# Performance work log

Hardware: AMD Instinct MI355X
Metric: run time of the kernel (lower is better)

## Reference

```python
import jax, jax.numpy as jnp
from jax import lax
import numpy as np

N_LAYER = 2
SEQ, BATCH, D = 4096, 32, 512


def setup_inputs() -> dict:
    key = jax.random.key(0)
    k1, k2, k3 = jax.random.split(key, 3)
    x = jax.random.normal(k1, (SEQ, BATCH, D), dtype=jnp.float32)
    # repo init: weight_ih ~ N(0, 0.01)
    W_ih = jax.random.normal(k2, (N_LAYER, D, D), dtype=jnp.float32) * 0.01
    # recurrent weight in [0,1) keeps the long ReLU recurrence bounded
    w_hh = jax.random.uniform(k3, (N_LAYER, D), dtype=jnp.float32)
    b_ih = jnp.zeros((N_LAYER, D), dtype=jnp.float32)
    return {"x": x, "W_ih": W_ih, "w_hh": w_hh, "b_ih": b_ih}


def _indrnn_layer(x, W, w, b):
    # x: (T, B, in), W: (H, in), w,b: (H,)
    proj = jnp.einsum('tbi,hi->tbh', x, W) + b  # one batched GEMM up front

    def step(h, p):
        h = jax.nn.relu(p + w * h)
        return h, h

    h0 = jnp.zeros((x.shape[1], W.shape[0]), dtype=x.dtype)
    hT, ys = lax.scan(step, h0, proj)
    return ys, hT


def reference(x, W_ih, w_hh, b_ih):
    hiddens = []
    out = x
    for l in range(W_ih.shape[0]):  # small fixed layer loop
        out, hT = _indrnn_layer(out, W_ih[l], w_hh[l], b_ih[l])
        hiddens.append(hT)
    h_n = jnp.stack(hiddens, axis=0)  # (n_layer, B, H)
    return out, h_n
```

## Files before the change

### kernel.cpp

```cpp
#include <hip/hip_runtime.h>

#define T_SEQ   4096
#define BATCH   32
#define DIM     512
#define MROWS   (T_SEQ * BATCH)
#define S_STRIDE (BATCH * DIM)
#define OUT_ELEMS ((size_t)T_SEQ * BATCH * DIM)
#define NCH     32
#define CLEN    (T_SEQ / NCH)
#define NCHAIN  (BATCH * DIM)
#define NWG     ((MROWS / 128) * (DIM / 128))

typedef __bf16 bf8_t __attribute__((ext_vector_type(8)));
typedef float  f4_t  __attribute__((ext_vector_type(4)));
typedef unsigned short u16x8 __attribute__((ext_vector_type(8)));
typedef __attribute__((address_space(1))) void gvoid_t;
typedef __attribute__((address_space(3))) void lvoid_t;

__device__ __forceinline__ unsigned short f2bf(float f) {
    unsigned int u = __float_as_uint(f);
    u += 0x7FFFu + ((u >> 16) & 1u);
    return (unsigned short)(u >> 16);
}
__device__ __forceinline__ float bf2f(unsigned short b) {
    return __uint_as_float(((unsigned int)b) << 16);
}

__global__ __launch_bounds__(256) void k_cvt(const float* __restrict__ in,
                                             unsigned short* __restrict__ out) {
    size_t i = ((size_t)blockIdx.x * 256 + threadIdx.x) * 8;
    float4 a = *reinterpret_cast<const float4*>(in + i);
    float4 b = *reinterpret_cast<const float4*>(in + i + 4);
    u16x8 o;
    o[0] = f2bf(a.x); o[1] = f2bf(a.y); o[2] = f2bf(a.z); o[3] = f2bf(a.w);
    o[4] = f2bf(b.x); o[5] = f2bf(b.y); o[6] = f2bf(b.z); o[7] = f2bf(b.w);
    *reinterpret_cast<u16x8*>(out + i) = o;
}

template <int AF32>
__global__ __launch_bounds__(256)
void k_gemm_bt(const void* __restrict__ Ap,
               const unsigned short* __restrict__ B,
               unsigned short* __restrict__ C) {
    __shared__ unsigned short As[128 * 32];
    __shared__ unsigned short Bs[128 * 32];

    const int tid  = threadIdx.x;
    const int lane = tid & 63;
    const int wv   = tid >> 6;
    const int wr   = wv >> 1;
    const int wc   = wv & 1;

    const int flat = blockIdx.x;
    const int s    = (flat & 7) * (NWG / 8) + (flat >> 3);
    const size_t gm = (size_t)(s >> 2) * 128;
    const int    gn = (s & 3) * 128;

    const int srow = tid >> 2;
    const int skk  = (tid & 3) * 8;

    f4_t acc[4][4] = {};

    const int l15 = lane & 15;
    const int lk  = (lane >> 4) * 8;

    for (int k0 = 0; k0 < 512; k0 += 32) {
#pragma unroll
        for (int i = 0; i < 2; ++i) {
            const unsigned short* gb = B + (size_t)(gn + i * 64 + srow) * 512 + k0 + skk;
            __builtin_amdgcn_global_load_lds((gvoid_t*)gb, (lvoid_t*)&Bs[i * 2048 + wv * 512], 16, 0, 0);
            if constexpr (AF32) {
                const float* ga = (const float*)Ap + (gm + (size_t)(i * 64 + srow)) * 512 + k0 + skk;
                float4 a0 = *reinterpret_cast<const float4*>(ga);
                float4 a1 = *reinterpret_cast<const float4*>(ga + 4);
                u16x8 o;
                o[0] = f2bf(a0.x); o[1] = f2bf(a0.y); o[2] = f2bf(a0.z); o[3] = f2bf(a0.w);
                o[4] = f2bf(a1.x); o[5] = f2bf(a1.y); o[6] = f2bf(a1.z); o[7] = f2bf(a1.w);
                *reinterpret_cast<u16x8*>(&As[i * 2048 + tid * 8]) = o;
            } else {
                const unsigned short* ga = (const unsigned short*)Ap + (gm + (size_t)(i * 64 + srow)) * 512 + k0 + skk;
                __builtin_amdgcn_global_load_lds((gvoid_t*)ga, (lvoid_t*)&As[i * 2048 + wv * 512], 16, 0, 0);
            }
        }
        __syncthreads();

        bf8_t af[4], bfz[4];
#pragma unroll
        for (int m = 0; m < 4; ++m)
            af[m] = *reinterpret_cast<const bf8_t*>(&As[(wr * 64 + m * 16 + l15) * 32 + lk]);
#pragma unroll
        for (int n = 0; n < 4; ++n)
            bfz[n] = *reinterpret_cast<const bf8_t*>(&Bs[(wc * 64 + n * 16 + l15) * 32 + lk]);
#pragma unroll
        for (int m = 0; m < 4; ++m)
#pragma unroll
            for (int n = 0; n < 4; ++n)
                acc[m][n] = __builtin_amdgcn_mfma_f32_16x16x32_bf16(af[m], bfz[n], acc[m][n], 0, 0, 0);
        __syncthreads();
    }

    const int crow0 = (lane >> 4) * 4;
#pragma unroll
    for (int m = 0; m < 4; ++m)
#pragma unroll
        for (int n = 0; n < 4; ++n) {
            const size_t row0 = gm + (size_t)(wr * 64 + m * 16 + crow0);
            const int    col  = gn + wc * 64 + n * 16 + l15;
#pragma unroll
            for (int r = 0; r < 4; ++r)
                C[(row0 + r) * 512 + col] = f2bf(acc[m][n][r]);
        }
}

__global__ __launch_bounds__(256)
void k_scan_p1(const unsigned short* __restrict__ q,
               const float* __restrict__ w_hh,
               const float* __restrict__ b_ih,
               float* __restrict__ Asum,
               float* __restrict__ Bsum) {
    const int g = (blockIdx.x & 63) * 256 + threadIdx.x;
    const int c = blockIdx.x >> 6;
    const float w  = w_hh[g & 511];
    const float bs = b_ih[g & 511];
    const unsigned short* p = q + (size_t)c * CLEN * S_STRIDE + g;

    float A = 0.f, Bv = 0.f;
    float s0[8], s1[8];
#pragma unroll
    for (int j = 0; j < 8; ++j) s0[j] = bf2f(p[(size_t)j * S_STRIDE]);
#pragma unroll
    for (int j = 0; j < 8; ++j) s1[j] = bf2f(p[(size_t)(8 + j) * S_STRIDE]);

    for (int j0 = 0; j0 < CLEN; j0 += 16) {
#pragma unroll
        for (int j = 0; j < 8; ++j) {
            float qv = s0[j] + bs;
            A  = fmaxf(fmaf(w, A, qv), 0.f);
            Bv = fmaf(w, Bv, qv);
        }
        if (j0 + 16 < CLEN) {
#pragma unroll
            for (int j = 0; j < 8; ++j) s0[j] = bf2f(p[(size_t)(j0 + 16 + j) * S_STRIDE]);
        }
#pragma unroll
        for (int j = 0; j < 8; ++j) {
            float qv = s1[j] + bs;
            A  = fmaxf(fmaf(w, A, qv), 0.f);
            Bv = fmaf(w, Bv, qv);
        }
        if (j0 + 24 < CLEN) {
#pragma unroll
            for (int j = 0; j < 8; ++j) s1[j] = bf2f(p[(size_t)(j0 + 24 + j) * S_STRIDE]);
        }
    }
    Asum[(size_t)c * NCHAIN + g] = A;
    Bsum[(size_t)c * NCHAIN + g] = Bv;
}

template <int MODE>
__global__ __launch_bounds__(256)
void k_scan_p2(const unsigned short* __restrict__ q,
               const float* __restrict__ w_hh,
               const float* __restrict__ b_ih,
               const float* __restrict__ Asum,
               const float* __restrict__ Bsum,
               float* __restrict__ of32,
               unsigned short* __restrict__ ob16,
               float* __restrict__ hT) {
    const int g = (blockIdx.x & 63) * 256 + threadIdx.x;
    const int c = blockIdx.x >> 6;
    const float w  = w_hh[g & 511];
    const float bs = b_ih[g & 511];

    float cw = w;
#pragma unroll
    for (int i = 0; i < 7; ++i) cw *= cw;
    float h = 0.f;
    for (int cc = 0; cc < c; ++cc)
        h = fmaxf(Asum[(size_t)cc * NCHAIN + g], fmaf(cw, h, Bsum[(size_t)cc * NCHAIN + g]));

    const size_t base = (size_t)c * CLEN * S_STRIDE + g;
    const unsigned short* p = q + base;

    float s0[8], s1[8];
#pragma unroll
    for (int j = 0; j < 8; ++j) s0[j] = bf2f(p[(size_t)j * S_STRIDE]);
#pragma unroll
    for (int j = 0; j < 8; ++j) s1[j] = bf2f(p[(size_t)(8 + j) * S_STRIDE]);

    for (int j0 = 0; j0 < CLEN; j0 += 16) {
#pragma unroll
        for (int j = 0; j < 8; ++j) {
            h = fmaxf(fmaf(w, h, s0[j] + bs), 0.f);
            const size_t idx = base + (size_t)(j0 + j) * S_STRIDE;
            if (MODE == 0) of32[idx] = h; else ob16[idx] = f2bf(h);
        }
        if (j0 + 16 < CLEN) {
#pragma unroll
            for (int j = 0; j < 8; ++j) s0[j] = bf2f(p[(size_t)(j0 + 16 + j) * S_STRIDE]);
        }
#pragma unroll
        for (int j = 0; j < 8; ++j) {
            h = fmaxf(fmaf(w, h, s1[j] + bs), 0.f);
            const size_t idx = base + (size_t)(j0 + 8 + j) * S_STRIDE;
            if (MODE == 0) of32[idx] = h; else ob16[idx] = f2bf(h);
        }
        if (j0 + 24 < CLEN) {
#pragma unroll
            for (int j = 0; j < 8; ++j) s1[j] = bf2f(p[(size_t)(j0 + 24 + j) * S_STRIDE]);
        }
    }
    if (c == NCH - 1) hT[g] = h;
}

extern "C" void kernel_launch(void* const* d_in, const int* in_sizes, int n_in,
                              void* d_out, int out_size, void* d_ws, size_t ws_size,
                              hipStream_t stream) {
    const float* x    = (const float*)d_in[0];
    const float* W_ih = (const float*)d_in[1];
    const float* w_hh = (const float*)d_in[2];
    const float* b_ih = (const float*)d_in[3];

    unsigned short* proj2 = (unsigned short*)d_ws;
    unsigned short* Wb    = proj2 + OUT_ELEMS;
    float* Asum = (float*)(Wb + 2 * 512 * 512);
    float* Bsum = Asum + (size_t)NCH * NCHAIN;

    unsigned short* proj1 = (unsigned short*)d_out;
    unsigned short* ys1   = proj1 + OUT_ELEMS;
    float* out = (float*)d_out;
    float* hT  = out + OUT_ELEMS;

    const int sgrid = 64 * NCH;

    k_cvt<<<524288 / 8 / 256, 256, 0, stream>>>(W_ih, Wb);
    k_gemm_bt<1><<<NWG, 256, 0, stream>>>(x, Wb, proj1);
    k_scan_p1<<<sgrid, 256, 0, stream>>>(proj1, w_hh, b_ih, Asum, Bsum);
    k_scan_p2<1><<<sgrid, 256, 0, stream>>>(proj1, w_hh, b_ih, Asum, Bsum,
                                            nullptr, ys1, hT);
    k_gemm_bt<0><<<NWG, 256, 0, stream>>>(ys1, Wb + 512 * 512, proj2);
    k_scan_p1<<<sgrid, 256, 0, stream>>>(proj2, w_hh + DIM, b_ih + DIM, Asum, Bsum);
    k_scan_p2<0><<<sgrid, 256, 0, stream>>>(proj2, w_hh + DIM, b_ih + DIM, Asum, Bsum,
                                            out, nullptr, hT + NCHAIN);
}
```

Measured before the change: 469.1 us.

## Restructure projection GEMM into full-N persistent tiles with double-buffered swizzled LDS

Replaces the 128x128-tile GEMM with 256 workgroups of 512 threads. Each workgroup computes full 512-wide output rows for four consecutive 128-row M tiles. The whole 512-column B slice for each K step is staged into 160KB of dynamic LDS, double-buffered with a prefetch distance of two and XOR-swizzled to avoid bank conflicts, with explicit vmcnt/lgkmcnt waits. This aims to cut redundant A reloads and barrier overhead and to overlap loads with MFMA, at the cost of heavy LDS use that limits occupancy and of fragile hand-tuned wait counts.

```diff
diff --git a/kernel.cpp b/kernel.cpp
--- a/kernel.cpp
+++ b/kernel.cpp
@@ -9,7 +9,13 @@
 #define NCH     32
 #define CLEN    (T_SEQ / NCH)
 #define NCHAIN  (BATCH * DIM)
-#define NWG     ((MROWS / 128) * (DIM / 128))
+
+#define NSTEP   32
+#define A0S     0
+#define A1S     8192
+#define B0S     16384
+#define B1S     49152
+#define GLDS_B  163840
 
 typedef __bf16 bf8_t __attribute__((ext_vector_type(8)));
 typedef float  f4_t  __attribute__((ext_vector_type(4)));
@@ -25,6 +31,9 @@
 __device__ __forceinline__ float bf2f(unsigned short b) {
     return __uint_as_float(((unsigned int)b) << 16);
 }
+
+#define VMC(n)  asm volatile("s_waitcnt vmcnt(" #n ")" ::: "memory")
+#define LGKM0   asm volatile("s_waitcnt lgkmcnt(0)" ::: "memory")
 
 __global__ __launch_bounds__(256) void k_cvt(const float* __restrict__ in,
                                              unsigned short* __restrict__ out) {
@@ -38,78 +47,159 @@
 }
 
 template <int AF32>
-__global__ __launch_bounds__(256)
-void k_gemm_bt(const void* __restrict__ Ap,
-               const unsigned short* __restrict__ B,
+__global__ __launch_bounds__(512, 2)
+void k_gemm_fn(const void* __restrict__ Ap,
+               const unsigned short* __restrict__ Bp,
                unsigned short* __restrict__ C) {
-    __shared__ unsigned short As[128 * 32];
-    __shared__ unsigned short Bs[128 * 32];
+    extern __shared__ unsigned short lds[];
 
     const int tid  = threadIdx.x;
     const int lane = tid & 63;
     const int wv   = tid >> 6;
-    const int wr   = wv >> 1;
-    const int wc   = wv & 1;
-
-    const int flat = blockIdx.x;
-    const int s    = (flat & 7) * (NWG / 8) + (flat >> 3);
-    const size_t gm = (size_t)(s >> 2) * 128;
-    const int    gn = (s & 3) * 128;
-
-    const int srow = tid >> 2;
-    const int skk  = (tid & 3) * 8;
-
-    f4_t acc[4][4] = {};
-
-    const int l15 = lane & 15;
-    const int lk  = (lane >> 4) * 8;
-
-    for (int k0 = 0; k0 < 512; k0 += 32) {
-#pragma unroll
-        for (int i = 0; i < 2; ++i) {
-            const unsigned short* gb = B + (size_t)(gn + i * 64 + srow) * 512 + k0 + skk;
-            __builtin_amdgcn_global_load_lds((gvoid_t*)gb, (lvoid_t*)&Bs[i * 2048 + wv * 512], 16, 0, 0);
+    const int l15  = lane & 15;
+    const int l16  = lane >> 4;
+    const int lj   = lane >> 3;
+    const int ss8  = lane & 7;
+    const int mbase = blockIdx.x * 4;
+
+    const unsigned short* Ab = (const unsigned short*)Ap;
+    const float*          Af = (const float*)Ap;
+
+    auto stageB = [&](int reg, int kt) {
+#pragma unroll
+        for (int j = 0; j < 8; ++j) {
+            const int r = j * 64 + wv * 8 + lj;
+            const unsigned short* src = Bp + (size_t)r * 512 + kt * 64 + (ss8 ^ lj) * 8;
+            unsigned short* dst = &lds[reg + (j * 64 + wv * 8) * 64];
+            __builtin_amdgcn_global_load_lds((gvoid_t*)src, (lvoid_t*)dst, 16, 0, 0);
+        }
+    };
+    auto stageA = [&](int reg, int kt, size_t gm) {
+#pragma unroll
+        for (int j = 0; j < 2; ++j) {
+            const int r = j * 64 + wv * 8 + lj;
+            const unsigned short* src = Ab + (gm + r) * 512 + kt * 64 + (ss8 ^ lj) * 8;
+            unsigned short* dst = &lds[reg + (j * 64 + wv * 8) * 64];
+            __builtin_amdgcn_global_load_lds((gvoid_t*)src, (lvoid_t*)dst, 16, 0, 0);
+        }
+    };
+    const int ra = tid >> 2, sg = tid & 3;
+    auto loadAf = [&](float4* h, int kt, size_t gm) {
+        const float* src = Af + (gm + ra) * 512 + kt * 64 + sg * 16;
+#pragma unroll
+        for (int q = 0; q < 4; ++q) h[q] = *reinterpret_cast<const float4*>(src + q * 4);
+    };
+    auto writeAf = [&](int reg, const float4* h) {
+        u16x8 o0, o1;
+        o0[0] = f2bf(h[0].x); o0[1] = f2bf(h[0].y); o0[2] = f2bf(h[0].z); o0[3] = f2bf(h[0].w);
+        o0[4] = f2bf(h[1].x); o0[5] = f2bf(h[1].y); o0[6] = f2bf(h[1].z); o0[7] = f2bf(h[1].w);
+        o1[0] = f2bf(h[2].x); o1[1] = f2bf(h[2].y); o1[2] = f2bf(h[2].z); o1[3] = f2bf(h[2].w);
+        o1[4] = f2bf(h[3].x); o1[5] = f2bf(h[3].y); o1[6] = f2bf(h[3].z); o1[7] = f2bf(h[3].w);
+        const int sl0 = (sg * 2) ^ (ra & 7), sl1 = (sg * 2 + 1) ^ (ra & 7);
+        *reinterpret_cast<u16x8*>(&lds[reg + ra * 64 + sl0 * 8]) = o0;
+        *reinterpret_cast<u16x8*>(&lds[reg + ra * 64 + sl1 * 8]) = o1;
+    };
+
+    f4_t  acc[8][4] = {};
+    float4 afP[4], afQ[4];
+
+    if constexpr (AF32) {
+        loadAf(afP, 0, (size_t)mbase * 128);
+        stageB(B0S, 0);
+        loadAf(afQ, 1, (size_t)mbase * 128);
+        stageB(B1S, 1);
+        VMC(20);
+        writeAf(A0S, afP);
+        LGKM0; __builtin_amdgcn_sched_barrier(0);
+        VMC(12);
+    } else {
+        stageA(A0S, 0, (size_t)mbase * 128);
+        stageB(B0S, 0);
+        stageA(A1S, 1, (size_t)mbase * 128);
+        stageB(B1S, 1);
+        VMC(10);
+    }
+    __builtin_amdgcn_s_barrier();
+
+#pragma unroll 2
+    for (int s = 0; s < NSTEP; ++s) {
+        const int Ar = (s & 1) ? A1S : A0S;
+        const int Br = (s & 1) ? B1S : B0S;
+
+        bf8_t bb[4][2];
+#pragma unroll
+        for (int n = 0; n < 4; ++n)
+#pragma unroll
+            for (int ks = 0; ks < 2; ++ks) {
+                const int c  = wv * 64 + n * 16 + l15;
+                const int sl = (ks * 4 + l16) ^ (l15 & 7);
+                bb[n][ks] = *reinterpret_cast<const bf8_t*>(
+                    (const char*)&lds[Br] + (size_t)c * 128 + sl * 16);
+            }
+#pragma unroll
+        for (int mh = 0; mh < 2; ++mh) {
+            bf8_t af[4][2];
+#pragma unroll
+            for (int m = 0; m < 4; ++m)
+#pragma unroll
+                for (int ks = 0; ks < 2; ++ks) {
+                    const int r  = (mh * 4 + m) * 16 + l15;
+                    const int sl = (ks * 4 + l16) ^ (l15 & 7);
+                    af[m][ks] = *reinterpret_cast<const bf8_t*>(
+                        (const char*)&lds[Ar] + (size_t)r * 128 + sl * 16);
+                }
+#pragma unroll
+            for (int m = 0; m < 4; ++m)
+#pragma unroll
+                for (int n = 0; n < 4; ++n)
+#pragma unroll
+                    for (int ks = 0; ks < 2; ++ks)
+                        acc[mh * 4 + m][n] = __builtin_amdgcn_mfma_f32_16x16x32_bf16(
+                            af[m][ks], bb[n][ks], acc[mh * 4 + m][n], 0, 0, 0);
+        }
+        __builtin_amdgcn_s_barrier();
+
+        const int s2 = s + 2;
+        if (s2 < NSTEP) {
+            const int    kt2 = s2 & 7;
+            const size_t gm2 = (size_t)(mbase + (s2 >> 3)) * 128;
             if constexpr (AF32) {
-                const float* ga = (const float*)Ap + (gm + (size_t)(i * 64 + srow)) * 512 + k0 + skk;
-                float4 a0 = *reinterpret_cast<const float4*>(ga);
-                float4 a1 = *reinterpret_cast<const float4*>(ga + 4);
-                u16x8 o;
-                o[0] = f2bf(a0.x); o[1] = f2bf(a0.y); o[2] = f2bf(a0.z); o[3] = f2bf(a0.w);
-                o[4] = f2bf(a1.x); o[5] = f2bf(a1.y); o[6] = f2bf(a1.z); o[7] = f2bf(a1.w);
-                *reinterpret_cast<u16x8*>(&As[i * 2048 + tid * 8]) = o;
+                if (s & 1) loadAf(afQ, kt2, gm2); else loadAf(afP, kt2, gm2);
+                stageB(Br, kt2);
+                VMC(12);
+                if (s & 1) writeAf(A0S, afP); else writeAf(A1S, afQ);
+                LGKM0; __builtin_amdgcn_sched_barrier(0);
             } else {
-                const unsigned short* ga = (const unsigned short*)Ap + (gm + (size_t)(i * 64 + srow)) * 512 + k0 + skk;
-                __builtin_amdgcn_global_load_lds((gvoid_t*)ga, (lvoid_t*)&As[i * 2048 + wv * 512], 16, 0, 0);
+                stageA(Ar, kt2, gm2);
+                stageB(Br, kt2);
+                VMC(10);
             }
-        }
-        __syncthreads();
-
-        bf8_t af[4], bfz[4];
-#pragma unroll
-        for (int m = 0; m < 4; ++m)
-            af[m] = *reinterpret_cast<const bf8_t*>(&As[(wr * 64 + m * 16 + l15) * 32 + lk]);
-#pragma unroll
-        for (int n = 0; n < 4; ++n)
-            bfz[n] = *reinterpret_cast<const bf8_t*>(&Bs[(wc * 64 + n * 16 + l15) * 32 + lk]);
-#pragma unroll
-        for (int m = 0; m < 4; ++m)
-#pragma unroll
-            for (int n = 0; n < 4; ++n)
-                acc[m][n] = __builtin_amdgcn_mfma_f32_16x16x32_bf16(af[m], bfz[n], acc[m][n], 0, 0, 0);
-        __syncthreads();
+        } else if (s == NSTEP - 2) {
+            if constexpr (AF32) {
+                VMC(8);
+                writeAf(A1S, afQ);
+                LGKM0; __builtin_amdgcn_sched_barrier(0);
+            }
+            VMC(0);
+        }
+        __builtin_amdgcn_s_barrier();
+
+        if ((s & 7) == 7) {
+            const size_t gmt  = (size_t)(mbase + (s >> 3)) * 128;
+            const int    crow0 = l16 * 4;
+#pragma unroll
+            for (int m = 0; m < 8; ++m)
+#pragma unroll
+                for (int n = 0; n < 4; ++n) {
+                    const size_t row0 = gmt + m * 16 + crow0;
+                    const int    col  = wv * 64 + n * 16 + l15;
+#pragma unroll
+                    for (int r = 0; r < 4; ++r)
+                        C[(row0 + r) * 512 + col] = f2bf(acc[m][n][r]);
+                    acc[m][n] = (f4_t){0.f, 0.f, 0.f, 0.f};
+                }
+        }
     }
-
-    const int crow0 = (lane >> 4) * 4;
-#pragma unroll
-    for (int m = 0; m < 4; ++m)
-#pragma unroll
-        for (int n = 0; n < 4; ++n) {
-            const size_t row0 = gm + (size_t)(wr * 64 + m * 16 + crow0);
-            const int    col  = gn + wc * 64 + n * 16 + l15;
-#pragma unroll
-            for (int r = 0; r < 4; ++r)
-                C[(row0 + r) * 512 + col] = f2bf(acc[m][n][r]);
-        }
 }
 
 __global__ __launch_bounds__(256)
@@ -221,6 +311,11 @@
     const float* w_hh = (const float*)d_in[2];
     const float* b_ih = (const float*)d_in[3];
 
+    hipFuncSetAttribute(reinterpret_cast<const void*>(&k_gemm_fn<1>),
+                        hipFuncAttributeMaxDynamicSharedMemorySize, GLDS_B);
+    hipFuncSetAttribute(reinterpret_cast<const void*>(&k_gemm_fn<0>),
+                        hipFuncAttributeMaxDynamicSharedMemorySize, GLDS_B);
+
     unsigned short* proj2 = (unsigned short*)d_ws;
     unsigned short* Wb    = proj2 + OUT_ELEMS;
     float* Asum = (float*)(Wb + 2 * 512 * 512);
@@ -234,11 +329,11 @@
     const int sgrid = 64 * NCH;
 
     k_cvt<<<524288 / 8 / 256, 256, 0, stream>>>(W_ih, Wb);
-    k_gemm_bt<1><<<NWG, 256, 0, stream>>>(x, Wb, proj1);
+    k_gemm_fn<1><<<256, 512, GLDS_B, stream>>>(x, Wb, proj1);
     k_scan_p1<<<sgrid, 256, 0, stream>>>(proj1, w_hh, b_ih, Asum, Bsum);
     k_scan_p2<1><<<sgrid, 256, 0, stream>>>(proj1, w_hh, b_ih, Asum, Bsum,
                                             nullptr, ys1, hT);
-    k_gemm_bt<0><<<NWG, 256, 0, stream>>>(ys1, Wb + 512 * 512, proj2);
+    k_gemm_fn<0><<<256, 512, GLDS_B, stream>>>(ys1, Wb + 512 * 512, proj2);
     k_scan_p1<<<sgrid, 256, 0, stream>>>(proj2, w_hh + DIM, b_ih + DIM, Asum, Bsum);
     k_scan_p2<0><<<sgrid, 256, 0, stream>>>(proj2, w_hh + DIM, b_ih + DIM, Asum, Bsum,
                                             out, nullptr, hT + NCHAIN);
```

New measurement: 422.3 us. 10.0% less time.

## Restructure projection GEMM with K=64 swizzled LDS tiles and persistent M-loop

Applied to the files above, without the earlier changes.

Replaces the GEMM kernel with one where each workgroup loops over four 128-row M tiles, giving 1024 workgroups instead of 4096. The K step grows from 32 to 64, which halves the barrier count per tile and issues two MFMAs per fragment pair. An XOR swizzle is added to the LDS layout to avoid bank conflicts on fragment reads. The fp32 input path now loads 32 floats per thread at once. The cost is double the LDS footprint and fewer workgroups, which could reduce occupancy and latency hiding.

```diff
diff --git a/kernel.cpp b/kernel.cpp
--- a/kernel.cpp
+++ b/kernel.cpp
@@ -9,7 +9,7 @@
 #define NCH     32
 #define CLEN    (T_SEQ / NCH)
 #define NCHAIN  (BATCH * DIM)
-#define NWG     ((MROWS / 128) * (DIM / 128))
+#define GNWG    1024
 
 typedef __bf16 bf8_t __attribute__((ext_vector_type(8)));
 typedef float  f4_t  __attribute__((ext_vector_type(4)));
@@ -39,77 +39,112 @@
 
 template <int AF32>
 __global__ __launch_bounds__(256)
-void k_gemm_bt(const void* __restrict__ Ap,
-               const unsigned short* __restrict__ B,
-               unsigned short* __restrict__ C) {
-    __shared__ unsigned short As[128 * 32];
-    __shared__ unsigned short Bs[128 * 32];
+void k_gemm_m97(const void* __restrict__ Ap,
+                const unsigned short* __restrict__ B,
+                unsigned short* __restrict__ C) {
+    __shared__ unsigned short As[128 * 64];
+    __shared__ unsigned short Bs[128 * 64];
 
     const int tid  = threadIdx.x;
     const int lane = tid & 63;
     const int wv   = tid >> 6;
     const int wr   = wv >> 1;
     const int wc   = wv & 1;
-
-    const int flat = blockIdx.x;
-    const int s    = (flat & 7) * (NWG / 8) + (flat >> 3);
-    const size_t gm = (size_t)(s >> 2) * 128;
-    const int    gn = (s & 3) * 128;
-
-    const int srow = tid >> 2;
-    const int skk  = (tid & 3) * 8;
-
-    f4_t acc[4][4] = {};
-
-    const int l15 = lane & 15;
-    const int lk  = (lane >> 4) * 8;
-
-    for (int k0 = 0; k0 < 512; k0 += 32) {
-#pragma unroll
-        for (int i = 0; i < 2; ++i) {
-            const unsigned short* gb = B + (size_t)(gn + i * 64 + srow) * 512 + k0 + skk;
-            __builtin_amdgcn_global_load_lds((gvoid_t*)gb, (lvoid_t*)&Bs[i * 2048 + wv * 512], 16, 0, 0);
+    const int l15  = lane & 15;
+    const int l16  = lane >> 4;
+
+    const int s  = (blockIdx.x & 7) * (GNWG / 8) + (blockIdx.x >> 3);
+    const int gn = (s & 3) * 128;
+    const size_t gmg = (size_t)(s >> 2) * 512;
+
+    const unsigned short* Ab = (const unsigned short*)Ap;
+    const float*          Af = (const float*)Ap;
+
+    auto stage16 = [&](const unsigned short* gb, size_t grow0,
+                       unsigned short* lbuf, int kt) {
+#pragma unroll
+        for (int j = 0; j < 4; ++j) {
+            const int r = j * 32 + wv * 8 + (lane >> 3);
+            const unsigned short* src =
+                gb + (grow0 + r) * 512 + kt * 64 + (((lane & 7) ^ (r & 7)) * 8);
+            __builtin_amdgcn_global_load_lds((gvoid_t*)src,
+                (lvoid_t*)&lbuf[(j * 32 + wv * 8) * 64], 16, 0, 0);
+        }
+    };
+
+    const int ar = tid >> 1;
+    const int ah = (tid & 1) * 4;
+
+    const int mtiles = 4;
+    for (int mt = 0; mt < mtiles; ++mt) {
+        const size_t gm = gmg + mt * 128;
+        f4_t acc[4][4] = {};
+
+        for (int kt = 0; kt < 8; ++kt) {
+            stage16(B, (size_t)gn, Bs, kt);
             if constexpr (AF32) {
-                const float* ga = (const float*)Ap + (gm + (size_t)(i * 64 + srow)) * 512 + k0 + skk;
-                float4 a0 = *reinterpret_cast<const float4*>(ga);
-                float4 a1 = *reinterpret_cast<const float4*>(ga + 4);
-                u16x8 o;
-                o[0] = f2bf(a0.x); o[1] = f2bf(a0.y); o[2] = f2bf(a0.z); o[3] = f2bf(a0.w);
-                o[4] = f2bf(a1.x); o[5] = f2bf(a1.y); o[6] = f2bf(a1.z); o[7] = f2bf(a1.w);
-                *reinterpret_cast<u16x8*>(&As[i * 2048 + tid * 8]) = o;
+                const float* src = Af + (gm + ar) * 512 + kt * 64 + ah * 8;
+                float4 f[8];
+#pragma unroll
+                for (int q = 0; q < 8; ++q)
+                    f[q] = *reinterpret_cast<const float4*>(src + q * 4);
+#pragma unroll
+                for (int q = 0; q < 4; ++q) {
+                    u16x8 o;
+                    o[0] = f2bf(f[2*q].x); o[1] = f2bf(f[2*q].y);
+                    o[2] = f2bf(f[2*q].z); o[3] = f2bf(f[2*q].w);
+                    o[4] = f2bf(f[2*q+1].x); o[5] = f2bf(f[2*q+1].y);
+                    o[6] = f2bf(f[2*q+1].z); o[7] = f2bf(f[2*q+1].w);
+                    *reinterpret_cast<u16x8*>(
+                        &As[ar * 64 + ((ah + q) ^ (ar & 7)) * 8]) = o;
+                }
             } else {
-                const unsigned short* ga = (const unsigned short*)Ap + (gm + (size_t)(i * 64 + srow)) * 512 + k0 + skk;
-                __builtin_amdgcn_global_load_lds((gvoid_t*)ga, (lvoid_t*)&As[i * 2048 + wv * 512], 16, 0, 0);
+                stage16(Ab, gm, As, kt);
             }
-        }
-        __syncthreads();
-
-        bf8_t af[4], bfz[4];
+            __syncthreads();
+
+            bf8_t af[4][2], bfz[4][2];
+#pragma unroll
+            for (int m = 0; m < 4; ++m)
+#pragma unroll
+                for (int ks = 0; ks < 2; ++ks) {
+                    const int r  = wr * 64 + m * 16 + l15;
+                    const int sl = (ks * 4 + l16) ^ (l15 & 7);
+                    af[m][ks] = *reinterpret_cast<const bf8_t*>(
+                        (const char*)As + r * 128 + sl * 16);
+                }
+#pragma unroll
+            for (int n = 0; n < 4; ++n)
+#pragma unroll
+                for (int ks = 0; ks < 2; ++ks) {
+                    const int r  = wc * 64 + n * 16 + l15;
+                    const int sl = (ks * 4 + l16) ^ (l15 & 7);
+                    bfz[n][ks] = *reinterpret_cast<const bf8_t*>(
+                        (const char*)Bs + r * 128 + sl * 16);
+                }
+#pragma unroll
+            for (int m = 0; m < 4; ++m)
+#pragma unroll
+                for (int n = 0; n < 4; ++n)
+#pragma unroll
+                    for (int ks = 0; ks < 2; ++ks)
+                        acc[m][n] = __builtin_amdgcn_mfma_f32_16x16x32_bf16(
+                            af[m][ks], bfz[n][ks], acc[m][n], 0, 0, 0);
+            __syncthreads();
+        }
+
+        const int crow0 = l16 * 4;
 #pragma unroll
         for (int m = 0; m < 4; ++m)
-            af[m] = *reinterpret_cast<const bf8_t*>(&As[(wr * 64 + m * 16 + l15) * 32 + lk]);
-#pragma unroll
-        for (int n = 0; n < 4; ++n)
-            bfz[n] = *reinterpret_cast<const bf8_t*>(&Bs[(wc * 64 + n * 16 + l15) * 32 + lk]);
-#pragma unroll
-        for (int m = 0; m < 4; ++m)
-#pragma unroll
-            for (int n = 0; n < 4; ++n)
-                acc[m][n] = __builtin_amdgcn_mfma_f32_16x16x32_bf16(af[m], bfz[n], acc[m][n], 0, 0, 0);
-        __syncthreads();
+#pragma unroll
+            for (int n = 0; n < 4; ++n) {
+                const size_t row0 = gm + (size_t)(wr * 64 + m * 16 + crow0);
+                const int    col  = gn + wc * 64 + n * 16 + l15;
+#pragma unroll
+                for (int r = 0; r < 4; ++r)
+                    C[(row0 + r) * 512 + col] = f2bf(acc[m][n][r]);
+            }
     }
-
-    const int crow0 = (lane >> 4) * 4;
-#pragma unroll
-    for (int m = 0; m < 4; ++m)
-#pragma unroll
-        for (int n = 0; n < 4; ++n) {
-            const size_t row0 = gm + (size_t)(wr * 64 + m * 16 + crow0);
-            const int    col  = gn + wc * 64 + n * 16 + l15;
-#pragma unroll
-            for (int r = 0; r < 4; ++r)
-                C[(row0 + r) * 512 + col] = f2bf(acc[m][n][r]);
-        }
 }
 
 __global__ __launch_bounds__(256)
@@ -234,11 +269,11 @@
     const int sgrid = 64 * NCH;
 
     k_cvt<<<524288 / 8 / 256, 256, 0, stream>>>(W_ih, Wb);
-    k_gemm_bt<1><<<NWG, 256, 0, stream>>>(x, Wb, proj1);
+    k_gemm_m97<1><<<GNWG, 256, 0, stream>>>(x, Wb, proj1);
     k_scan_p1<<<sgrid, 256, 0, stream>>>(proj1, w_hh, b_ih, Asum, Bsum);
     k_scan_p2<1><<<sgrid, 256, 0, stream>>>(proj1, w_hh, b_ih, Asum, Bsum,
                                             nullptr, ys1, hT);
-    k_gemm_bt<0><<<NWG, 256, 0, stream>>>(ys1, Wb + 512 * 512, proj2);
+    k_gemm_m97<0><<<GNWG, 256, 0, stream>>>(ys1, Wb + 512 * 512, proj2);
     k_scan_p1<<<sgrid, 256, 0, stream>>>(proj2, w_hh + DIM, b_ih + DIM, Asum, Bsum);
     k_scan_p2<0><<<sgrid, 256, 0, stream>>>(proj2, w_hh + DIM, b_ih + DIM, Asum, Bsum,
                                             out, nullptr, hT + NCHAIN);
```

Result: slower. 514.5 us (+9.7%).

## Triple-buffer GEMM LDS tiles with manual waitcnt pipelining and XOR swizzle

Applied to the files above, without the earlier changes.

Rewrites the projection GEMM so that global-to-LDS loads for the tile two k-steps ahead are issued before the MFMA work on the current tile, using three LDS buffers, explicit vmcnt/lgkmcnt waits and a single barrier per step. For the fp32 input path, the next A tile is loaded into registers and converted while compute proceeds. LDS columns are XOR-swizzled to reduce bank conflicts on the MFMA fragment reads, and launch bounds request 3 blocks per CU. The aim is to hide global memory latency in these memory-heavy GEMMs. In exchange it uses more LDS and registers, and hand-written waitcnt values risk subtle races.

```diff
diff --git a/kernel.cpp b/kernel.cpp
--- a/kernel.cpp
+++ b/kernel.cpp
@@ -9,7 +9,7 @@
 #define NCH     32
 #define CLEN    (T_SEQ / NCH)
 #define NCHAIN  (BATCH * DIM)
-#define NWG     ((MROWS / 128) * (DIM / 128))
+#define GNWG    4096
 
 typedef __bf16 bf8_t __attribute__((ext_vector_type(8)));
 typedef float  f4_t  __attribute__((ext_vector_type(4)));
@@ -25,6 +25,12 @@
 __device__ __forceinline__ float bf2f(unsigned short b) {
     return __uint_as_float(((unsigned int)b) << 16);
 }
+
+#define VMC0 asm volatile("s_waitcnt vmcnt(0)" ::: "memory")
+#define VMC4 asm volatile("s_waitcnt vmcnt(4)" ::: "memory")
+#define VMC6 asm volatile("s_waitcnt vmcnt(6)" ::: "memory")
+#define VMC8 asm volatile("s_waitcnt vmcnt(8)" ::: "memory")
+#define LGKM0 asm volatile("s_waitcnt lgkmcnt(0)" ::: "memory")
 
 __global__ __launch_bounds__(256) void k_cvt(const float* __restrict__ in,
                                              unsigned short* __restrict__ out) {
@@ -38,68 +44,133 @@
 }
 
 template <int AF32>
-__global__ __launch_bounds__(256)
-void k_gemm_bt(const void* __restrict__ Ap,
-               const unsigned short* __restrict__ B,
+__global__ __launch_bounds__(256, 3)
+void k_gemm_tb(const void* __restrict__ Ap,
+               const unsigned short* __restrict__ Bp,
                unsigned short* __restrict__ C) {
-    __shared__ unsigned short As[128 * 32];
-    __shared__ unsigned short Bs[128 * 32];
+    __shared__ unsigned short As[3][4096];
+    __shared__ unsigned short Bs[3][4096];
 
     const int tid  = threadIdx.x;
     const int lane = tid & 63;
     const int wv   = tid >> 6;
     const int wr   = wv >> 1;
     const int wc   = wv & 1;
-
-    const int flat = blockIdx.x;
-    const int s    = (flat & 7) * (NWG / 8) + (flat >> 3);
-    const size_t gm = (size_t)(s >> 2) * 128;
-    const int    gn = (s & 3) * 128;
-
-    const int srow = tid >> 2;
-    const int skk  = (tid & 3) * 8;
+    const int l15  = lane & 15;
+    const int l16q = lane >> 4;
+    const int swl  = (l15 & 3) ^ ((l15 >> 2) & 3);
+
+    const int r0 = tid >> 2,         sl0 = tid & 3;
+    const int r1 = (256 + tid) >> 2;
+    const int ko0 = (sl0 ^ ((r0 & 3) ^ ((r0 >> 2) & 3))) * 8;
+    const int ko1 = (sl0 ^ ((r1 & 3) ^ ((r1 >> 2) & 3))) * 8;
+
+    const int s_  = (blockIdx.x & 7) * (GNWG / 8) + (blockIdx.x >> 3);
+    const int gn  = (s_ & 3) * 128;
+    const size_t gm = (size_t)(s_ >> 2) * 128;
+
+    const unsigned short* Ab = (const unsigned short*)Ap;
+    const float*          Af = (const float*)Ap;
+
+    auto stageTo = [&](unsigned short* buf, const unsigned short* gb,
+                       size_t grow0, int kt) {
+        __builtin_amdgcn_global_load_lds(
+            (gvoid_t*)(gb + (grow0 + r0) * 512 + kt * 32 + ko0),
+            (lvoid_t*)&buf[(wv * 64) * 8], 16, 0, 0);
+        __builtin_amdgcn_global_load_lds(
+            (gvoid_t*)(gb + (grow0 + r1) * 512 + kt * 32 + ko1),
+            (lvoid_t*)&buf[(256 + wv * 64) * 8], 16, 0, 0);
+    };
+
+#define LOADAF(S, kt) do {                                                   \
+        const float* pa_ = Af + (gm + r0) * 512 + (kt) * 32 + ko0;           \
+        const float* pb_ = Af + (gm + r1) * 512 + (kt) * 32 + ko1;           \
+        S[0] = *reinterpret_cast<const float4*>(pa_);                        \
+        S[1] = *reinterpret_cast<const float4*>(pa_ + 4);                    \
+        S[2] = *reinterpret_cast<const float4*>(pb_);                        \
+        S[3] = *reinterpret_cast<const float4*>(pb_ + 4);                    \
+    } while (0)
+
+#define WRITEAF(S, buf) do {                                                 \
+        u16x8 oa_, ob_;                                                      \
+        oa_[0]=f2bf(S[0].x); oa_[1]=f2bf(S[0].y); oa_[2]=f2bf(S[0].z); oa_[3]=f2bf(S[0].w); \
+        oa_[4]=f2bf(S[1].x); oa_[5]=f2bf(S[1].y); oa_[6]=f2bf(S[1].z); oa_[7]=f2bf(S[1].w); \
+        ob_[0]=f2bf(S[2].x); ob_[1]=f2bf(S[2].y); ob_[2]=f2bf(S[2].z); ob_[3]=f2bf(S[2].w); \
+        ob_[4]=f2bf(S[3].x); ob_[5]=f2bf(S[3].y); ob_[6]=f2bf(S[3].z); ob_[7]=f2bf(S[3].w); \
+        *reinterpret_cast<u16x8*>(&(buf)[tid * 8])         = oa_;            \
+        *reinterpret_cast<u16x8*>(&(buf)[(256 + tid) * 8]) = ob_;            \
+    } while (0)
+
+#define COMPUTE(bA, bB) do {                                                 \
+        bf8_t af_[4], bf_[4];                                                \
+        _Pragma("unroll")                                                    \
+        for (int m = 0; m < 4; ++m)                                          \
+            af_[m] = *reinterpret_cast<const bf8_t*>(                        \
+                &(bA)[(wr * 64 + m * 16 + l15) * 32 + (l16q ^ swl) * 8]);    \
+        _Pragma("unroll")                                                    \
+        for (int n = 0; n < 4; ++n)                                          \
+            bf_[n] = *reinterpret_cast<const bf8_t*>(                        \
+                &(bB)[(wc * 64 + n * 16 + l15) * 32 + (l16q ^ swl) * 8]);    \
+        _Pragma("unroll")                                                    \
+        for (int m = 0; m < 4; ++m)                                          \
+            _Pragma("unroll")                                                \
+            for (int n = 0; n < 4; ++n)                                      \
+                acc[m][n] = __builtin_amdgcn_mfma_f32_16x16x32_bf16(         \
+                    af_[m], bf_[n], acc[m][n], 0, 0, 0);                     \
+    } while (0)
 
     f4_t acc[4][4] = {};
-
-    const int l15 = lane & 15;
-    const int lk  = (lane >> 4) * 8;
-
-    for (int k0 = 0; k0 < 512; k0 += 32) {
-#pragma unroll
-        for (int i = 0; i < 2; ++i) {
-            const unsigned short* gb = B + (size_t)(gn + i * 64 + srow) * 512 + k0 + skk;
-            __builtin_amdgcn_global_load_lds((gvoid_t*)gb, (lvoid_t*)&Bs[i * 2048 + wv * 512], 16, 0, 0);
-            if constexpr (AF32) {
-                const float* ga = (const float*)Ap + (gm + (size_t)(i * 64 + srow)) * 512 + k0 + skk;
-                float4 a0 = *reinterpret_cast<const float4*>(ga);
-                float4 a1 = *reinterpret_cast<const float4*>(ga + 4);
-                u16x8 o;
-                o[0] = f2bf(a0.x); o[1] = f2bf(a0.y); o[2] = f2bf(a0.z); o[3] = f2bf(a0.w);
-                o[4] = f2bf(a1.x); o[5] = f2bf(a1.y); o[6] = f2bf(a1.z); o[7] = f2bf(a1.w);
-                *reinterpret_cast<u16x8*>(&As[i * 2048 + tid * 8]) = o;
-            } else {
-                const unsigned short* ga = (const unsigned short*)Ap + (gm + (size_t)(i * 64 + srow)) * 512 + k0 + skk;
-                __builtin_amdgcn_global_load_lds((gvoid_t*)ga, (lvoid_t*)&As[i * 2048 + wv * 512], 16, 0, 0);
-            }
-        }
-        __syncthreads();
-
-        bf8_t af[4], bfz[4];
-#pragma unroll
-        for (int m = 0; m < 4; ++m)
-            af[m] = *reinterpret_cast<const bf8_t*>(&As[(wr * 64 + m * 16 + l15) * 32 + lk]);
-#pragma unroll
-        for (int n = 0; n < 4; ++n)
-            bfz[n] = *reinterpret_cast<const bf8_t*>(&Bs[(wc * 64 + n * 16 + l15) * 32 + lk]);
-#pragma unroll
-        for (int m = 0; m < 4; ++m)
-#pragma unroll
-            for (int n = 0; n < 4; ++n)
-                acc[m][n] = __builtin_amdgcn_mfma_f32_16x16x32_bf16(af[m], bfz[n], acc[m][n], 0, 0, 0);
-        __syncthreads();
+    float4 P[4], Q[4];
+
+    unsigned short *cA = As[0], *cB = Bs[0];
+    unsigned short *nA = As[1], *nB = Bs[1];
+    unsigned short *fA = As[2], *fB = Bs[2];
+
+    if constexpr (AF32) {
+        LOADAF(P, 0); stageTo(cB, Bp, (size_t)gn, 0);
+        LOADAF(Q, 1); stageTo(nB, Bp, (size_t)gn, 1);
+        VMC8;
+        WRITEAF(P, cA);
+        VMC6;
+        LGKM0;
+    } else {
+        stageTo(cA, Ab, gm, 0); stageTo(cB, Bp, (size_t)gn, 0);
+        stageTo(nA, Ab, gm, 1); stageTo(nB, Bp, (size_t)gn, 1);
+        VMC4;
     }
-
-    const int crow0 = (lane >> 4) * 4;
+    __builtin_amdgcn_s_barrier();
+
+#define GSTEP(s, SI, SW_) do {                                               \
+        if ((s) + 2 < 16) {                                                  \
+            stageTo(fB, Bp, (size_t)gn, (s) + 2);                            \
+            if constexpr (AF32) { LOADAF(SI, (s) + 2); }                     \
+            else stageTo(fA, Ab, gm, (s) + 2);                               \
+        }                                                                    \
+        COMPUTE(cA, cB);                                                     \
+        if ((s) + 2 < 16) { if constexpr (AF32) { VMC6; } else { VMC4; } }   \
+        else if ((s) == 14) { VMC0; }                                        \
+        if constexpr (AF32) {                                                \
+            if ((s) + 1 < 16) { WRITEAF(SW_, nA); LGKM0; }                   \
+        }                                                                    \
+        if ((s) < 15) __builtin_amdgcn_s_barrier();                          \
+    } while (0)
+
+    for (int s = 0; s < 16; s += 2) {
+        GSTEP(s, P, Q);
+        { unsigned short* t;
+          t = cA; cA = nA; nA = fA; fA = t;
+          t = cB; cB = nB; nB = fB; fB = t; }
+        GSTEP(s + 1, Q, P);
+        { unsigned short* t;
+          t = cA; cA = nA; nA = fA; fA = t;
+          t = cB; cB = nB; nB = fB; fB = t; }
+    }
+#undef GSTEP
+#undef COMPUTE
+#undef WRITEAF
+#undef LOADAF
+
+    const int crow0 = l16q * 4;
 #pragma unroll
     for (int m = 0; m < 4; ++m)
 #pragma unroll
@@ -234,11 +305,11 @@
     const int sgrid = 64 * NCH;
 
     k_cvt<<<524288 / 8 / 256, 256, 0, stream>>>(W_ih, Wb);
-    k_gemm_bt<1><<<NWG, 256, 0, stream>>>(x, Wb, proj1);
+    k_gemm_tb<1><<<GNWG, 256, 0, stream>>>(x, Wb, proj1);
     k_scan_p1<<<sgrid, 256, 0, stream>>>(proj1, w_hh, b_ih, Asum, Bsum);
     k_scan_p2<1><<<sgrid, 256, 0, stream>>>(proj1, w_hh, b_ih, Asum, Bsum,
                                             nullptr, ys1, hT);
-    k_gemm_bt<0><<<NWG, 256, 0, stream>>>(ys1, Wb + 512 * 512, proj2);
+    k_gemm_tb<0><<<GNWG, 256, 0, stream>>>(ys1, Wb + 512 * 512, proj2);
     k_scan_p1<<<sgrid, 256, 0, stream>>>(proj2, w_hh + DIM, b_ih + DIM, Asum, Bsum);
     k_scan_p2<0><<<sgrid, 256, 0, stream>>>(proj2, w_hh + DIM, b_ih + DIM, Asum, Bsum,
                                             out, nullptr, hT + NCHAIN);
```

Measured after the change: 460.4 us. About the same (-1.8%).
